# Kernel tuning notes

Measured on AMD Instinct MI355X. Metric: run time of the kernel, lower is better.

## Reference

```python
import jax, jax.numpy as jnp
import numpy as np

BLOCK_SIZE = 256
N_EMBD = 384
HEAD_SIZE = 384
B = 256
T = 256


def setup_inputs() -> dict:
    key = jax.random.key(0)
    kx, kk, kq, kv = jax.random.split(key, 4)
    scale = 1.0 / np.sqrt(N_EMBD)
    x = jax.random.normal(kx, (B, T, N_EMBD), dtype=jnp.float32)
    Wk = jax.random.normal(kk, (HEAD_SIZE, N_EMBD), dtype=jnp.float32) * scale
    Wq = jax.random.normal(kq, (HEAD_SIZE, N_EMBD), dtype=jnp.float32) * scale
    Wv = jax.random.normal(kv, (HEAD_SIZE, N_EMBD), dtype=jnp.float32) * scale
    return {"x": x, "Wk": Wk, "Wq": Wq, "Wv": Wv}


def reference(x, Wk, Wq, Wv):
    # Single-head causal self-attention; equals forward_with_cache at prefill
    # (fresh cache, cache_index=0, T tokens) and forward_no_cache.
    # Linear layers are bias-free: y = x @ W.T
    k = jnp.einsum('btc,hc->bth', x, Wk)  # [B,T,H]
    q = jnp.einsum('btc,hc->bth', x, Wq)
    v = jnp.einsum('btc,hc->bth', x, Wv)
    inv_sqrt_hs = jnp.asarray(HEAD_SIZE, x.dtype) ** -0.5
    wei = jnp.einsum('bth,bsh->bts', q, k) * inv_sqrt_hs  # [B,T,T]
    causal = jnp.tril(jnp.ones((T, T), dtype=bool))
    wei = jnp.where(causal, wei, jnp.asarray(-jnp.inf, wei.dtype))
    wei = jax.nn.softmax(wei, axis=-1)
    # dropout is identity in eval mode
    out = jnp.einsum('bts,bsh->bth', wei, v)  # [B,T,H]
    return out
```

## Files before the change

kernel.cpp:

```cpp
#include <hip/hip_runtime.h>

#define B_ 256
#define T_ 256
#define C_ 384
#define H_ 384

typedef float f4 __attribute__((ext_vector_type(4)));
typedef float f32x4 __attribute__((ext_vector_type(4)));
typedef short bf8 __attribute__((ext_vector_type(8)));
typedef short s8v __attribute__((ext_vector_type(8)));
typedef short s4v __attribute__((ext_vector_type(4)));

__device__ __forceinline__ short f2bf(float f) {
  unsigned u = __builtin_bit_cast(unsigned, f);
  u += 0x7FFFu + ((u >> 16) & 1u);
  return (short)(u >> 16);
}

__device__ __forceinline__ void gload_lds16(const void* g, void* l) {
  __builtin_amdgcn_global_load_lds(
      (const __attribute__((address_space(1))) unsigned int*)g,
      (__attribute__((address_space(3))) unsigned int*)l, 16, 0, 0);
}

__global__ __launch_bounds__(256) void convert_kernel(
    const float* __restrict__ x, const float* __restrict__ wk,
    const float* __restrict__ wq, const float* __restrict__ wv,
    short* __restrict__ xb, short* __restrict__ wb) {
  const int NXG = (B_ * T_ * C_) / 8;
  const int NWG = (H_ * C_) / 8;
  const int total = NXG + 3 * NWG;
  for (int g = blockIdx.x * 256 + threadIdx.x; g < total; g += gridDim.x * 256) {
    const float* src;
    short* dst;
    if (g < NXG) {
      src = x + (size_t)g * 8;
      dst = xb + (size_t)g * 8;
    } else {
      int h = g - NXG;
      int wsel = h / NWG;
      int o = h - wsel * NWG;
      const float* wp = wsel == 0 ? wk : (wsel == 1 ? wq : wv);
      src = wp + (size_t)o * 8;
      dst = wb + (size_t)wsel * (H_ * C_) + (size_t)o * 8;
    }
    f4 f0 = *(const f4*)src;
    f4 f1 = *(const f4*)(src + 4);
    s8v r;
    r[0] = f2bf(f0[0]); r[1] = f2bf(f0[1]); r[2] = f2bf(f0[2]); r[3] = f2bf(f0[3]);
    r[4] = f2bf(f1[0]); r[5] = f2bf(f1[1]); r[6] = f2bf(f1[2]); r[7] = f2bf(f1[3]);
    *(s8v*)dst = r;
  }
}

__global__ __launch_bounds__(256) void proj_gemm(
    const short* __restrict__ xb, const short* __restrict__ wb,
    short* __restrict__ kb, short* __restrict__ qbuf, short* __restrict__ vt) {
  __shared__ __align__(16) short lA[128 * 64];
  __shared__ __align__(16) short lB[128 * 64];
  const int tid = threadIdx.x;
  const int nb = blockIdx.x % 9;
  const int mb = blockIdx.x / 9;
  const int m0 = mb * 128, gn0 = nb * 128;
  const int w = tid >> 6, l = tid & 63;
  const int wr = w >> 1, wc = w & 1;
  f32x4 acc[4][4] = {};
  for (int kc = 0; kc < 6; ++kc) {
    const int k0 = kc * 64;
#pragma unroll
    for (int j = 0; j < 4; ++j) {
      const int flat = j * 256 + tid;
      const int row = flat >> 3, colg = (flat & 7) * 8;
      gload_lds16(xb + (size_t)(m0 + row) * C_ + k0 + colg, (char*)lA + flat * 16);
      gload_lds16(wb + (size_t)(gn0 + row) * C_ + k0 + colg, (char*)lB + flat * 16);
    }
    __syncthreads();
#pragma unroll
    for (int ks = 0; ks < 2; ++ks) {
      const int kk = ks * 32 + (l >> 4) * 8;
      bf8 av[4], bv[4];
#pragma unroll
      for (int mt = 0; mt < 4; ++mt)
        av[mt] = *(const bf8*)&lA[(wr * 64 + mt * 16 + (l & 15)) * 64 + kk];
#pragma unroll
      for (int nt = 0; nt < 4; ++nt)
        bv[nt] = *(const bf8*)&lB[(wc * 64 + nt * 16 + (l & 15)) * 64 + kk];
#pragma unroll
      for (int mt = 0; mt < 4; ++mt)
#pragma unroll
        for (int nt = 0; nt < 4; ++nt)
          acc[mt][nt] = __builtin_amdgcn_mfma_f32_16x16x32_bf16(
              av[mt], bv[nt], acc[mt][nt], 0, 0, 0);
    }
    __syncthreads();
  }
  const int proj = nb / 3;
  const int gcb = (nb % 3) * 128 + wc * 64 + (l & 15);
  const int tok0 = m0 + wr * 64 + ((l >> 4) * 4);
  if (proj < 2) {
    short* dst = proj == 0 ? kb : qbuf;
#pragma unroll
    for (int mt = 0; mt < 4; ++mt)
#pragma unroll
      for (int nt = 0; nt < 4; ++nt)
#pragma unroll
        for (int r = 0; r < 4; ++r)
          dst[(size_t)(tok0 + mt * 16 + r) * H_ + gcb + nt * 16] =
              f2bf(acc[mt][nt][r]);
  } else {
    const int bb = tok0 >> 8;
    const int tl0 = tok0 & 255;
#pragma unroll
    for (int mt = 0; mt < 4; ++mt)
#pragma unroll
      for (int nt = 0; nt < 4; ++nt) {
        s4v pk;
        pk[0] = f2bf(acc[mt][nt][0]); pk[1] = f2bf(acc[mt][nt][1]);
        pk[2] = f2bf(acc[mt][nt][2]); pk[3] = f2bf(acc[mt][nt][3]);
        *(s4v*)&vt[(size_t)bb * (H_ * T_) + (size_t)(gcb + nt * 16) * T_ +
                   tl0 + mt * 16] = pk;
      }
  }
}

__global__ __launch_bounds__(256) void attn_kernel(
    const short* __restrict__ qbuf, const short* __restrict__ kb,
    const short* __restrict__ vt, float* __restrict__ out) {
  __shared__ __align__(16) char smem[40960];
  short* Kl = (short*)smem;
  short* Ql = (short*)(smem + 32768);
  short* Pl = (short*)smem;
  const int b = blockIdx.x >> 2;
  const int qi = blockIdx.x & 3;
  const int t0 = qi * 64;
  const int SKV = t0 + 64;
  const int ntile = SKV >> 4;
  const int tid = threadIdx.x;
  const int w = tid >> 6, l = tid & 63;
  f32x4 sa[16] = {};
  for (int hc = 0; hc < 6; ++hc) {
    const int h0 = hc * 64;
#pragma unroll
    for (int j = 0; j < 2; ++j) {
      const int flat = j * 256 + tid;
      const int row = flat >> 3, colg = (flat & 7) * 8;
      gload_lds16(qbuf + (size_t)(b * T_ + t0 + row) * H_ + h0 + colg,
                  (char*)Ql + flat * 16);
    }
    const int kiss = SKV >> 5;
    for (int j = 0; j < kiss; ++j) {
      const int flat = j * 256 + tid;
      const int row = flat >> 3, colg = (flat & 7) * 8;
      gload_lds16(kb + (size_t)(b * T_ + row) * H_ + h0 + colg,
                  (char*)Kl + flat * 16);
    }
    __syncthreads();
#pragma unroll
    for (int ks = 0; ks < 2; ++ks) {
      const int kk = ks * 32 + (l >> 4) * 8;
      bf8 av = *(const bf8*)&Ql[(w * 16 + (l & 15)) * 64 + kk];
#pragma unroll
      for (int nt = 0; nt < 16; ++nt)
        if (nt < ntile) {
          bf8 bv = *(const bf8*)&Kl[(nt * 16 + (l & 15)) * 64 + kk];
          sa[nt] = __builtin_amdgcn_mfma_f32_16x16x32_bf16(av, bv, sa[nt], 0, 0, 0);
        }
    }
    __syncthreads();
  }
  const float scale = 0.05103103630798287f;
  const int rbl = w * 16 + (l >> 4) * 4;
#pragma unroll
  for (int r = 0; r < 4; ++r) {
    const int trow = t0 + rbl + r;
    float vv[16];
    float m = -3.0e38f;
#pragma unroll
    for (int nt = 0; nt < 16; ++nt)
      if (nt < ntile) {
        const int col = nt * 16 + (l & 15);
        float v = sa[nt][r] * scale;
        if (col > trow) v = -3.0e38f;
        vv[nt] = v;
        m = fmaxf(m, v);
      }
    m = fmaxf(m, __shfl_xor(m, 1));
    m = fmaxf(m, __shfl_xor(m, 2));
    m = fmaxf(m, __shfl_xor(m, 4));
    m = fmaxf(m, __shfl_xor(m, 8));
    float s = 0.f;
#pragma unroll
    for (int nt = 0; nt < 16; ++nt)
      if (nt < ntile) {
        vv[nt] = __expf(vv[nt] - m);
        s += vv[nt];
      }
    s += __shfl_xor(s, 1);
    s += __shfl_xor(s, 2);
    s += __shfl_xor(s, 4);
    s += __shfl_xor(s, 8);
    const float inv = 1.0f / s;
#pragma unroll
    for (int nt = 0; nt < 16; ++nt)
      if (nt < ntile)
        Pl[(rbl + r) * 256 + nt * 16 + (l & 15)] = f2bf(vv[nt] * inv);
  }
  __syncthreads();
  f32x4 o[4][6] = {};
  const int nks = SKV >> 5;
  for (int ks = 0; ks < nks; ++ks) {
    const int kk = ks * 32 + (l >> 4) * 8;
    bf8 av[4];
#pragma unroll
    for (int mt = 0; mt < 4; ++mt)
      av[mt] = *(const bf8*)&Pl[(mt * 16 + (l & 15)) * 256 + kk];
#pragma unroll
    for (int nt = 0; nt < 6; ++nt) {
      const int d = w * 96 + nt * 16 + (l & 15);
      bf8 bv = *(const bf8*)&vt[(size_t)b * (H_ * T_) + (size_t)d * T_ + kk];
#pragma unroll
      for (int mt = 0; mt < 4; ++mt)
        o[mt][nt] = __builtin_amdgcn_mfma_f32_16x16x32_bf16(av[mt], bv, o[mt][nt], 0, 0, 0);
    }
  }
#pragma unroll
  for (int mt = 0; mt < 4; ++mt) {
    const int tok = b * T_ + t0 + mt * 16 + (l >> 4) * 4;
#pragma unroll
    for (int nt = 0; nt < 6; ++nt) {
      const int d = w * 96 + nt * 16 + (l & 15);
#pragma unroll
      for (int r = 0; r < 4; ++r)
        out[(size_t)(tok + r) * H_ + d] = o[mt][nt][r];
    }
  }
}

extern "C" void kernel_launch(void* const* d_in, const int* in_sizes, int n_in,
                              void* d_out, int out_size, void* d_ws, size_t ws_size,
                              hipStream_t stream) {
  (void)in_sizes; (void)n_in; (void)out_size; (void)ws_size;
  const float* x = (const float*)d_in[0];
  const float* wk = (const float*)d_in[1];
  const float* wq = (const float*)d_in[2];
  const float* wv = (const float*)d_in[3];
  float* out = (float*)d_out;
  char* ws = (char*)d_ws;
  const size_t SZ = (size_t)B_ * T_ * H_ * 2;
  short* kbuf = (short*)ws;
  short* qbuf = (short*)(ws + SZ);
  short* vt   = (short*)(ws + 2 * SZ);
  short* xb = (short*)d_out;
  short* wb = (short*)((char*)d_out + SZ);
  convert_kernel<<<2048, 256, 0, stream>>>(x, wk, wq, wv, xb, wb);
  proj_gemm<<<4608, 256, 0, stream>>>(xb, wb, kbuf, qbuf, vt);
  attn_kernel<<<1024, 256, 0, stream>>>(qbuf, kbuf, vt, out);
}
```

Measured before the change: 370.0 us.

## XOR-swizzle LDS tiles to avoid bank conflicts and remap GEMM block order

Applies an XOR swizzle on the 16-byte column groups of the LDS tiles in the projection GEMM and the attention QK^T and PV stages, so that the 16 lanes reading rows with a 128-byte or 512-byte stride land in different LDS banks. The projection GEMM also remaps block IDs so that consecutive blocks are spread across eight groups, which changes L2 locality across XCDs. This adds some index arithmetic, and any mismatch between the write and read swizzles would corrupt results.

```diff
diff --git a/kernel.cpp b/kernel.cpp
--- a/kernel.cpp
+++ b/kernel.cpp
@@ -59,8 +59,11 @@
   __shared__ __align__(16) short lA[128 * 64];
   __shared__ __align__(16) short lB[128 * 64];
   const int tid = threadIdx.x;
-  const int nb = blockIdx.x % 9;
-  const int mb = blockIdx.x / 9;
+  const int cpx = 4608 / 8;
+  const int bid = blockIdx.x;
+  const int swz = (bid & 7) * cpx + (bid >> 3);
+  const int nb = swz % 9;
+  const int mb = swz / 9;
   const int m0 = mb * 128, gn0 = nb * 128;
   const int w = tid >> 6, l = tid & 63;
   const int wr = w >> 1, wc = w & 1;
@@ -70,21 +73,26 @@
 #pragma unroll
     for (int j = 0; j < 4; ++j) {
       const int flat = j * 256 + tid;
-      const int row = flat >> 3, colg = (flat & 7) * 8;
+      const int row = flat >> 3;
+      const int colg = ((flat & 7) ^ (row & 7)) * 8;
       gload_lds16(xb + (size_t)(m0 + row) * C_ + k0 + colg, (char*)lA + flat * 16);
       gload_lds16(wb + (size_t)(gn0 + row) * C_ + k0 + colg, (char*)lB + flat * 16);
     }
     __syncthreads();
 #pragma unroll
     for (int ks = 0; ks < 2; ++ks) {
-      const int kk = ks * 32 + (l >> 4) * 8;
+      const int kg = ks * 4 + (l >> 4);
       bf8 av[4], bv[4];
 #pragma unroll
-      for (int mt = 0; mt < 4; ++mt)
-        av[mt] = *(const bf8*)&lA[(wr * 64 + mt * 16 + (l & 15)) * 64 + kk];
-#pragma unroll
-      for (int nt = 0; nt < 4; ++nt)
-        bv[nt] = *(const bf8*)&lB[(wc * 64 + nt * 16 + (l & 15)) * 64 + kk];
+      for (int mt = 0; mt < 4; ++mt) {
+        const int ra = wr * 64 + mt * 16 + (l & 15);
+        av[mt] = *(const bf8*)&lA[ra * 64 + ((kg ^ (ra & 7)) << 3)];
+      }
+#pragma unroll
+      for (int nt = 0; nt < 4; ++nt) {
+        const int rb = wc * 64 + nt * 16 + (l & 15);
+        bv[nt] = *(const bf8*)&lB[rb * 64 + ((kg ^ (rb & 7)) << 3)];
+      }
 #pragma unroll
       for (int mt = 0; mt < 4; ++mt)
 #pragma unroll
@@ -143,26 +151,30 @@
 #pragma unroll
     for (int j = 0; j < 2; ++j) {
       const int flat = j * 256 + tid;
-      const int row = flat >> 3, colg = (flat & 7) * 8;
+      const int row = flat >> 3;
+      const int colg = ((flat & 7) ^ (row & 7)) * 8;
       gload_lds16(qbuf + (size_t)(b * T_ + t0 + row) * H_ + h0 + colg,
                   (char*)Ql + flat * 16);
     }
     const int kiss = SKV >> 5;
     for (int j = 0; j < kiss; ++j) {
       const int flat = j * 256 + tid;
-      const int row = flat >> 3, colg = (flat & 7) * 8;
+      const int row = flat >> 3;
+      const int colg = ((flat & 7) ^ (row & 7)) * 8;
       gload_lds16(kb + (size_t)(b * T_ + row) * H_ + h0 + colg,
                   (char*)Kl + flat * 16);
     }
     __syncthreads();
 #pragma unroll
     for (int ks = 0; ks < 2; ++ks) {
-      const int kk = ks * 32 + (l >> 4) * 8;
-      bf8 av = *(const bf8*)&Ql[(w * 16 + (l & 15)) * 64 + kk];
+      const int kg = ks * 4 + (l >> 4);
+      const int rq = w * 16 + (l & 15);
+      bf8 av = *(const bf8*)&Ql[rq * 64 + ((kg ^ (rq & 7)) << 3)];
 #pragma unroll
       for (int nt = 0; nt < 16; ++nt)
         if (nt < ntile) {
-          bf8 bv = *(const bf8*)&Kl[(nt * 16 + (l & 15)) * 64 + kk];
+          const int rk = nt * 16 + (l & 15);
+          bf8 bv = *(const bf8*)&Kl[rk * 64 + ((kg ^ (rk & 7)) << 3)];
           sa[nt] = __builtin_amdgcn_mfma_f32_16x16x32_bf16(av, bv, sa[nt], 0, 0, 0);
         }
     }
@@ -172,7 +184,8 @@
   const int rbl = w * 16 + (l >> 4) * 4;
 #pragma unroll
   for (int r = 0; r < 4; ++r) {
-    const int trow = t0 + rbl + r;
+    const int prow = rbl + r;
+    const int trow = t0 + prow;
     float vv[16];
     float m = -3.0e38f;
 #pragma unroll
@@ -200,10 +213,13 @@
     s += __shfl_xor(s, 4);
     s += __shfl_xor(s, 8);
     const float inv = 1.0f / s;
+    const int sw = (prow & 7) << 3;
 #pragma unroll
     for (int nt = 0; nt < 16; ++nt)
-      if (nt < ntile)
-        Pl[(rbl + r) * 256 + nt * 16 + (l & 15)] = f2bf(vv[nt] * inv);
+      if (nt < ntile) {
+        const int col = nt * 16 + (l & 15);
+        Pl[prow * 256 + (col ^ sw)] = f2bf(vv[nt] * inv);
+      }
   }
   __syncthreads();
   f32x4 o[4][6] = {};
@@ -212,8 +228,10 @@
     const int kk = ks * 32 + (l >> 4) * 8;
     bf8 av[4];
 #pragma unroll
-    for (int mt = 0; mt < 4; ++mt)
-      av[mt] = *(const bf8*)&Pl[(mt * 16 + (l & 15)) * 256 + kk];
+    for (int mt = 0; mt < 4; ++mt) {
+      const int rp = mt * 16 + (l & 15);
+      av[mt] = *(const bf8*)&Pl[rp * 256 + (kk ^ ((rp & 7) << 3))];
+    }
 #pragma unroll
     for (int nt = 0; nt < 6; ++nt) {
       const int d = w * 96 + nt * 16 + (l & 15);
```

Result: faster. 339.6 us (-8.2%).
